# Optimization experiments

Hardware: AMD Instinct MI355X
Metric: run time of the kernel (lower is better)

## Reference

```python
import jax, jax.numpy as jnp
import numpy as np

D_MODEL = 2048
N_HEADS = 16
D_HEAD = 128
B = 2
S = 2048


def setup_inputs() -> dict:
    key = jax.random.key(0)
    ks = jax.random.split(key, 9)
    sc_in = 1.0 / np.sqrt(D_MODEL)
    sc_hd = 1.0 / np.sqrt(N_HEADS * D_HEAD)
    return {
        "x": jax.random.normal(ks[0], (B, S, D_MODEL), dtype=jnp.float32),
        "Wq": jax.random.normal(ks[1], (D_MODEL, N_HEADS * D_HEAD), dtype=jnp.float32) * sc_in,
        "bq": jax.random.normal(ks[2], (N_HEADS * D_HEAD,), dtype=jnp.float32) * 0.01,
        "Wk": jax.random.normal(ks[3], (D_MODEL, N_HEADS * D_HEAD), dtype=jnp.float32) * sc_in,
        "bk": jax.random.normal(ks[4], (N_HEADS * D_HEAD,), dtype=jnp.float32) * 0.01,
        "Wv": jax.random.normal(ks[5], (D_MODEL, N_HEADS * D_HEAD), dtype=jnp.float32) * sc_in,
        "bv": jax.random.normal(ks[6], (N_HEADS * D_HEAD,), dtype=jnp.float32) * 0.01,
        "Wo": jax.random.normal(ks[7], (N_HEADS * D_HEAD, D_MODEL), dtype=jnp.float32) * sc_hd,
        "bo": jax.random.normal(ks[8], (D_MODEL,), dtype=jnp.float32) * 0.01,
    }


def reference(x, Wq, bq, Wk, bk, Wv, bv, Wo, bo):
    b, s, _ = x.shape
    # projections -> [b, s, h, d] -> [b, h, s, d]
    q = (x @ Wq + bq).reshape(b, s, N_HEADS, D_HEAD).transpose(0, 2, 1, 3)
    k = (x @ Wk + bk).reshape(b, s, N_HEADS, D_HEAD).transpose(0, 2, 1, 3)
    v = (x @ Wv + bv).reshape(b, s, N_HEADS, D_HEAD).transpose(0, 2, 1, 3)
    scale = 1.0 / jnp.sqrt(jnp.asarray(D_HEAD, dtype=x.dtype))
    scores = jnp.einsum("bhsd,bhtd->bhst", q, k) * scale  # [b,h,s,s]
    causal = jnp.triu(jnp.ones((s, s), dtype=bool), k=1)
    scores = jnp.where(causal, jnp.asarray(-jnp.inf, dtype=scores.dtype), scores)
    attn = jax.nn.softmax(scores, axis=-1)
    ctx = jnp.einsum("bhst,bhtd->bhsd", attn, v)  # [b,h,s,d]
    ctx = ctx.transpose(0, 2, 1, 3).reshape(b, s, N_HEADS * D_HEAD)
    return ctx @ Wo + bo
```

## Files before the change

### kernel.cpp

```cpp
#include <hip/hip_runtime.h>
#include <hip/hip_bf16.h>
#include <stdint.h>

#define S_LEN  2048
#define DMODEL 2048
#define NHEADS 16
#define DHEAD  128
#define NBATCH 2
#define MROWS  (NBATCH * S_LEN)

typedef __bf16 bf16_t;
typedef __bf16 bf16x8 __attribute__((ext_vector_type(8)));
typedef float  f32x4  __attribute__((ext_vector_type(4)));
typedef float  f32x16 __attribute__((ext_vector_type(16)));

#define MFMA_BF16(A, B, C) __builtin_amdgcn_mfma_f32_16x16x32_bf16((A), (B), (C), 0, 0, 0)
#define MFMA32(A, B, C)    __builtin_amdgcn_mfma_f32_32x32x16_bf16((A), (B), (C), 0, 0, 0)

__device__ __forceinline__ void gload_lds16(const void* g, void* l) {
  __builtin_amdgcn_global_load_lds(
      (__attribute__((address_space(1))) uint32_t*)(uintptr_t)g,
      (__attribute__((address_space(3))) uint32_t*)l,
      16, 0, 0);
}

__device__ __forceinline__ unsigned pk2(float lo, float hi) {
  const unsigned short a = __builtin_bit_cast(unsigned short, (bf16_t)lo);
  const unsigned short b = __builtin_bit_cast(unsigned short, (bf16_t)hi);
  return (unsigned)a | ((unsigned)b << 16);
}

__global__ __launch_bounds__(256) void cast_kernel(const float* __restrict__ X,
                                                   bf16_t* __restrict__ Xb) {
  const int i = blockIdx.x * 256 + threadIdx.x;
  const f32x4 a = ((const f32x4*)X)[2 * i];
  const f32x4 b = ((const f32x4*)X)[2 * i + 1];
  bf16x8 o;
#pragma unroll
  for (int j = 0; j < 4; ++j) { o[j] = (bf16_t)a[j]; o[j + 4] = (bf16_t)b[j]; }
  ((bf16x8*)Xb)[i] = o;
}

__global__ __launch_bounds__(256) void transpose_cast(
    const float* __restrict__ W0, const float* __restrict__ W1,
    const float* __restrict__ W2, const float* __restrict__ W3,
    bf16_t* __restrict__ T0, bf16_t* __restrict__ T1,
    bf16_t* __restrict__ T2, bf16_t* __restrict__ T3) {
  const float* W; bf16_t* T;
  switch (blockIdx.z) {
    case 0:  W = W0; T = T0; break;
    case 1:  W = W1; T = T1; break;
    case 2:  W = W2; T = T2; break;
    default: W = W3; T = T3; break;
  }
  __shared__ float tile[64][65];
  const int r0 = blockIdx.y * 64;
  const int c0 = blockIdx.x * 64;
  const int tx = threadIdx.x & 63;
  const int ty = threadIdx.x >> 6;
#pragma unroll
  for (int i = 0; i < 16; ++i) {
    const int r = ty + i * 4;
    tile[r][tx] = W[(size_t)(r0 + r) * DMODEL + c0 + tx];
  }
  __syncthreads();
#pragma unroll
  for (int i = 0; i < 16; ++i) {
    const int r = ty + i * 4;
    T[(size_t)(c0 + r) * DMODEL + r0 + tx] = (bf16_t)tile[tx][r];
  }
}

__global__ __launch_bounds__(256) void transpose_v(const bf16_t* __restrict__ V,
                                                   bf16_t* __restrict__ VT) {
  __shared__ bf16_t tile[64 * 64];
  const int bh = blockIdx.z;
  const int s0 = blockIdx.x * 64;
  const int d0 = blockIdx.y * 64;
  const bf16_t* src = V + ((size_t)bh * S_LEN + s0) * DHEAD + d0;
#pragma unroll
  for (int i = 0; i < 2; ++i) {
    const int v = threadIdx.x + i * 256;
    const int r = v >> 3, ch = v & 7;
    *(bf16x8*)&tile[r * 64 + ((ch ^ ((r >> 3) & 7)) << 3)] =
        *(const bf16x8*)(src + (size_t)r * DHEAD + ch * 8);
  }
  __syncthreads();
  bf16_t* dst = VT + ((size_t)bh * DHEAD + d0) * S_LEN + s0;
#pragma unroll
  for (int i = 0; i < 2; ++i) {
    const int v = threadIdx.x + i * 256;
    const int d = v >> 3, j = v & 7;
    bf16x8 o;
#pragma unroll
    for (int e = 0; e < 8; ++e) {
      const int row = j * 8 + e;
      o[e] = tile[row * 64 + (((d >> 3) ^ j) << 3) + (d & 7)];
    }
    *(bf16x8*)(dst + (size_t)d * S_LEN + j * 8) = o;
  }
}

template <int MODE>
__device__ __forceinline__ void gemm_body(const bf16_t* __restrict__ A,
                                          const bf16_t* __restrict__ Bt,
                                          const float* __restrict__ bias,
                                          void* __restrict__ out) {
  __shared__ bf16_t lds[128 * 32 * 2];
  const int tid  = threadIdx.x;
  const int lane = tid & 63;
  const int w    = tid >> 6;
  const int g    = lane >> 4;
  const int l16  = lane & 15;
  const int m0   = blockIdx.y * 128;
  const int n0   = blockIdx.x * 128;
  const int wm   = w >> 1, wn = w & 1;

  f32x4 acc[4][4];
#pragma unroll
  for (int i = 0; i < 4; ++i)
#pragma unroll
    for (int j = 0; j < 4; ++j) acc[i][j] = (f32x4){0.f, 0.f, 0.f, 0.f};

  const bf16_t* src   = (w < 2) ? A : Bt;
  const int rowbase   = (w < 2) ? m0 : n0;
  char* ldsst         = (char*)lds + (w >= 2 ? 8192 : 0);
  const char* lA      = (const char*)lds;
  const char* lB      = (const char*)lds + 8192;

  for (int kt = 0; kt < DMODEL; kt += 32) {
#pragma unroll
    for (int it = 0; it < 4; ++it) {
      const int c   = (w & 1) * 256 + it * 64 + lane;
      const int row = c >> 2;
      const int q4  = (c & 3) ^ (row & 3);
      gload_lds16(src + (size_t)(rowbase + row) * DMODEL + kt + q4 * 8,
                  ldsst + ((w & 1) * 256 + it * 64) * 16);
    }
    asm volatile("s_waitcnt vmcnt(0)" ::: "memory");
    __syncthreads();

    bf16x8 af[4], bfr[4];
#pragma unroll
    for (int i = 0; i < 4; ++i) {
      const int row = wm * 64 + i * 16 + l16;
      af[i] = *(const bf16x8*)(lA + row * 64 + ((g * 16) ^ ((row & 3) << 4)));
    }
#pragma unroll
    for (int j = 0; j < 4; ++j) {
      const int row = wn * 64 + j * 16 + l16;
      bfr[j] = *(const bf16x8*)(lB + row * 64 + ((g * 16) ^ ((row & 3) << 4)));
    }
#pragma unroll
    for (int i = 0; i < 4; ++i)
#pragma unroll
      for (int j = 0; j < 4; ++j)
        acc[i][j] = MFMA_BF16(af[i], bfr[j], acc[i][j]);
    __syncthreads();
  }

#pragma unroll
  for (int i = 0; i < 4; ++i) {
#pragma unroll
    for (int j = 0; j < 4; ++j) {
      const int n    = n0 + wn * 64 + j * 16 + l16;
      const float bb = bias[n];
#pragma unroll
      for (int r = 0; r < 4; ++r) {
        const int m   = m0 + wm * 64 + i * 16 + g * 4 + r;
        const float v = acc[i][j][r] + bb;
        if (MODE == 0) {
          const int b = m >> 11, s = m & (S_LEN - 1);
          const int h = n >> 7,  d = n & (DHEAD - 1);
          ((bf16_t*)out)[((size_t)(b * NHEADS + h) * S_LEN + s) * DHEAD + d] = (bf16_t)v;
        } else {
          ((float*)out)[(size_t)m * DMODEL + n] = v;
        }
      }
    }
  }
}

__global__ __launch_bounds__(256, 2) void gemm_qkv(
    const bf16_t* __restrict__ Xb,
    const bf16_t* __restrict__ WqT, const bf16_t* __restrict__ WkT,
    const bf16_t* __restrict__ WvT,
    const float* __restrict__ bq, const float* __restrict__ bk,
    const float* __restrict__ bv,
    bf16_t* __restrict__ Qg, bf16_t* __restrict__ Kg, bf16_t* __restrict__ Vg) {
  const bf16_t* Bt; const float* bias; bf16_t* out;
  if (blockIdx.z == 0)      { Bt = WqT; bias = bq; out = Qg; }
  else if (blockIdx.z == 1) { Bt = WkT; bias = bk; out = Kg; }
  else                      { Bt = WvT; bias = bv; out = Vg; }
  gemm_body<0>(Xb, Bt, bias, out);
}

__global__ __launch_bounds__(256, 2) void gemm_out(
    const bf16_t* __restrict__ Ctx, const bf16_t* __restrict__ WoT,
    const float* __restrict__ bo, float* __restrict__ out) {
  gemm_body<1>(Ctx, WoT, bo, out);
}

#define KLDS_BYTES (64 * 272)
#define VLDS_BYTES (128 * 144)
#define BUF_BYTES  (KLDS_BYTES + VLDS_BYTES)

__global__ __launch_bounds__(256, 2) void attn_kernel(
    const bf16_t* __restrict__ Qg, const bf16_t* __restrict__ Kg,
    const bf16_t* __restrict__ VTg, bf16_t* __restrict__ ctx) {
  __shared__ __align__(16) char ldsbuf[2][BUF_BYTES];
  __shared__ float lbuf[4][32];

  const int tid  = threadIdx.x;
  const int lane = tid & 63;
  const int w    = tid >> 6;
  const int l31  = lane & 31;
  const int hi   = lane >> 5;

  const int id   = blockIdx.x;
  const int bh   = id & 31;
  const int jraw = id >> 5;
  const int j    = (jraw < 8) ? jraw : 23 - jraw;
  const int q0   = j * 128;
  const int qw   = q0 + w * 32;
  const int tq   = (qw + 31) >> 6;
  const int NT   = (q0 + 128) >> 6;

  const size_t bho = (size_t)bh * S_LEN * DHEAD;
  const bf16_t* Qb  = Qg + bho;
  const bf16_t* Kb  = Kg + bho;
  const bf16_t* VTb = VTg + bho;

  bf16x8 qreg[8];
#pragma unroll
  for (int s = 0; s < 8; ++s)
    qreg[s] = *(const bf16x8*)(Qb + (size_t)(qw + l31) * DHEAD + s * 16 + hi * 8);

  f32x16 oacc[4];
#pragma unroll
  for (int d0 = 0; d0 < 4; ++d0)
#pragma unroll
    for (int e = 0; e < 16; ++e) oacc[d0][e] = 0.f;

  float m = -1e30f, lsum = 0.f;
  const float sc2 = 0.12751751135f;

  bf16x8 kst[4], vst[4];
#pragma unroll
  for (int i = 0; i < 4; ++i) {
    const int c = tid + i * 256;
    kst[i] = *(const bf16x8*)(Kb + (size_t)(c >> 4) * DHEAD + (c & 15) * 8);
    vst[i] = *(const bf16x8*)(VTb + (size_t)(c >> 3) * S_LEN + (c & 7) * 8);
  }
#pragma unroll
  for (int i = 0; i < 4; ++i) {
    const int c  = tid + i * 256;
    const int kr = c >> 4, kc = c & 15;
    *(bf16x8*)(ldsbuf[0] + kr * 272 + ((kc ^ ((kr >> 3) & 3)) << 4)) = kst[i];
    const int vr = c >> 3, vc = c & 7;
    *(bf16x8*)(ldsbuf[0] + KLDS_BYTES + vr * 144 + ((vc ^ ((vr >> 3) & 3)) << 4)) = vst[i];
  }
  __syncthreads();

  for (int t = 0; t < NT; ++t) {
    const int kt = t << 6;
    const char* bK = ldsbuf[t & 1];
    const char* bV = bK + KLDS_BYTES;
    const bool hn = (t + 1 < NT);
    if (hn) {
#pragma unroll
      for (int i = 0; i < 4; ++i) {
        const int c = tid + i * 256;
        kst[i] = *(const bf16x8*)(Kb + (size_t)(kt + 64 + (c >> 4)) * DHEAD + (c & 15) * 8);
        vst[i] = *(const bf16x8*)(VTb + (size_t)(c >> 3) * S_LEN + kt + 64 + (c & 7) * 8);
      }
    }

    if (t <= tq) {
      f32x16 stt[2];
#pragma unroll
      for (int kh = 0; kh < 2; ++kh)
#pragma unroll
        for (int e = 0; e < 16; ++e) stt[kh][e] = 0.f;
#pragma unroll
      for (int kh = 0; kh < 2; ++kh) {
        const int row = kh * 32 + l31;
        const char* rb = bK + row * 272;
        const int swz = ((row >> 3) & 3) << 4;
#pragma unroll
        for (int s = 0; s < 8; ++s) {
          const bf16x8 kf = *(const bf16x8*)(rb + ((((s << 1) | hi) << 4) ^ swz));
          stt[kh] = MFMA32(kf, qreg[s], stt[kh]);
        }
      }
      if (t == tq) {
        const int qg = qw + l31;
#pragma unroll
        for (int kh = 0; kh < 2; ++kh)
#pragma unroll
          for (int r = 0; r < 16; ++r) {
            const int kv = kt + kh * 32 + (r & 3) + 8 * (r >> 2) + 4 * hi;
            stt[kh][r] = (kv > qg) ? -1e30f : stt[kh][r];
          }
      }
      float pm = stt[0][0];
#pragma unroll
      for (int kh = 0; kh < 2; ++kh)
#pragma unroll
        for (int r = 0; r < 16; ++r)
          if (kh | r) pm = fmaxf(pm, stt[kh][r]);
      pm = fmaxf(pm, __shfl_xor(pm, 32));
      const float pmax = pm * sc2;
      if (!__all(pmax <= m + 8.f)) {
        const float mn   = fmaxf(m, pmax);
        const float corr = __builtin_amdgcn_exp2f(m - mn);
        m = mn;
        lsum *= corr;
        if (!hi) lbuf[w][l31] = corr;
#pragma unroll
        for (int r = 0; r < 16; ++r) {
          const float cr = lbuf[w][(r & 3) + 8 * (r >> 2) + 4 * hi];
#pragma unroll
          for (int d0 = 0; d0 < 4; ++d0) oacc[d0][r] *= cr;
        }
      }
      float rs = 0.f;
#pragma unroll
      for (int kh = 0; kh < 2; ++kh)
#pragma unroll
        for (int r = 0; r < 16; ++r) {
          const float p = __builtin_amdgcn_exp2f(__builtin_fmaf(stt[kh][r], sc2, -m));
          stt[kh][r] = p;
          rs += p;
        }
      rs += __shfl_xor(rs, 32);
      lsum += rs;
      unsigned pw_[2][8];
#pragma unroll
      for (int kh = 0; kh < 2; ++kh)
#pragma unroll
        for (int jj = 0; jj < 8; ++jj)
          pw_[kh][jj] = pk2(stt[kh][2 * jj], stt[kh][2 * jj + 1]);
      bf16x8 pa[4];
#pragma unroll
      for (int kh = 0; kh < 2; ++kh)
#pragma unroll
        for (int c2 = 0; c2 < 2; ++c2) {
          const unsigned o0 = pw_[kh][4 * c2 + 0], o1 = pw_[kh][4 * c2 + 1];
          const unsigned o2 = pw_[kh][4 * c2 + 2], o3 = pw_[kh][4 * c2 + 3];
          const unsigned p0 = (unsigned)__shfl_xor((int)o0, 32);
          const unsigned p1 = (unsigned)__shfl_xor((int)o1, 32);
          const unsigned p2 = (unsigned)__shfl_xor((int)o2, 32);
          const unsigned p3 = (unsigned)__shfl_xor((int)o3, 32);
          union { unsigned u[4]; bf16x8 v; } uu;
          uu.u[0] = hi ? p2 : o0;
          uu.u[1] = hi ? p3 : o1;
          uu.u[2] = hi ? o2 : p0;
          uu.u[3] = hi ? o3 : p1;
          pa[2 * kh + c2] = uu.v;
        }
#pragma unroll
      for (int d0 = 0; d0 < 4; ++d0) {
        const int row = d0 * 32 + l31;
        const char* rb = bV + row * 144;
        const int swz = ((row >> 3) & 3) << 4;
#pragma unroll
        for (int ks = 0; ks < 4; ++ks) {
          const bf16x8 vb = *(const bf16x8*)(rb + ((((ks << 1) | hi) << 4) ^ swz));
          oacc[d0] = MFMA32(pa[ks], vb, oacc[d0]);
        }
      }
    }
    __syncthreads();
    if (hn) {
      char* nB = ldsbuf[(t + 1) & 1];
#pragma unroll
      for (int i = 0; i < 4; ++i) {
        const int c  = tid + i * 256;
        const int kr = c >> 4, kc = c & 15;
        *(bf16x8*)(nB + kr * 272 + ((kc ^ ((kr >> 3) & 3)) << 4)) = kst[i];
        const int vr = c >> 3, vc = c & 7;
        *(bf16x8*)(nB + KLDS_BYTES + vr * 144 + ((vc ^ ((vr >> 3) & 3)) << 4)) = vst[i];
      }
    }
    __syncthreads();
  }

  if (!hi) lbuf[w][l31] = 1.0f / lsum;
  const int b = bh >> 4, h = bh & 15;
#pragma unroll
  for (int r = 0; r < 16; ++r) {
    const int cro = (r & 3) + 8 * (r >> 2) + 4 * hi;
    const float li = lbuf[w][cro];
    const size_t base = ((size_t)(b * S_LEN + qw + cro)) * DMODEL + h * DHEAD;
#pragma unroll
    for (int d0 = 0; d0 < 4; ++d0)
      ctx[base + d0 * 32 + l31] = (bf16_t)(oacc[d0][r] * li);
  }
}

extern "C" void kernel_launch(void* const* d_in, const int* in_sizes, int n_in,
                              void* d_out, int out_size, void* d_ws, size_t ws_size,
                              hipStream_t stream) {
  const float* x  = (const float*)d_in[0];
  const float* Wq = (const float*)d_in[1];
  const float* bq = (const float*)d_in[2];
  const float* Wk = (const float*)d_in[3];
  const float* bk = (const float*)d_in[4];
  const float* Wv = (const float*)d_in[5];
  const float* bv = (const float*)d_in[6];
  const float* Wo = (const float*)d_in[7];
  const float* bo = (const float*)d_in[8];

  char* ws = (char*)d_ws;
  const size_t MB = 1ull << 20;
  bf16_t* Xb  = (bf16_t*)(ws + 0);
  bf16_t* VTg = (bf16_t*)(ws + 0);
  bf16_t* WqT = (bf16_t*)(ws + 16 * MB);
  bf16_t* WkT = (bf16_t*)(ws + 24 * MB);
  bf16_t* WvT = (bf16_t*)(ws + 32 * MB);
  bf16_t* WoT = (bf16_t*)(ws + 40 * MB);
  bf16_t* Qg  = (bf16_t*)(ws + 48 * MB);
  bf16_t* Kg  = (bf16_t*)(ws + 64 * MB);
  bf16_t* Vg  = (bf16_t*)(ws + 80 * MB);
  bf16_t* Ctx = (bf16_t*)(ws + 96 * MB);
  if (ws_size < 112 * MB) return;

  cast_kernel<<<dim3(MROWS * DMODEL / (256 * 8)), 256, 0, stream>>>(x, Xb);
  transpose_cast<<<dim3(32, 32, 4), 256, 0, stream>>>(Wq, Wk, Wv, Wo, WqT, WkT, WvT, WoT);
  gemm_qkv<<<dim3(DMODEL / 128, MROWS / 128, 3), 256, 0, stream>>>(
      Xb, WqT, WkT, WvT, bq, bk, bv, Qg, Kg, Vg);
  transpose_v<<<dim3(32, 2, 32), 256, 0, stream>>>(Vg, VTg);
  attn_kernel<<<dim3(512), 256, 0, stream>>>(Qg, Kg, VTg, Ctx);
  gemm_out<<<dim3(DMODEL / 128, MROWS / 128), 256, 0, stream>>>(Ctx, WoT, bo, (float*)d_out);
}
```

Measured before the change: 266.0 us.

## Rewrite projection GEMMs as 8-wave 128x256 tiles with double-buffered LDS prefetch

Replaces the single-buffered 128x128, 4-wave GEMM body with an 8-wave kernel covering 128x256 output tiles at K-step 64. Global-to-LDS loads for the next tile are issued between the two MFMA phases, so memory traffic overlaps compute; raw s_barrier calls and explicit waitcnt replace the full syncthreads, and s_setprio raises priority around the MFMA blocks. The wider tile cuts re-reads of A. In exchange it uses 96KB of LDS per block, which limits occupancy to about one block per CU, and relies on hand-tuned vmcnt counts being correct.

```diff
diff --git a/kernel.cpp b/kernel.cpp
--- a/kernel.cpp
+++ b/kernel.cpp
@@ -102,19 +102,20 @@
 }
 
 template <int MODE>
-__device__ __forceinline__ void gemm_body(const bf16_t* __restrict__ A,
-                                          const bf16_t* __restrict__ Bt,
-                                          const float* __restrict__ bias,
-                                          void* __restrict__ out) {
-  __shared__ bf16_t lds[128 * 32 * 2];
+__device__ __forceinline__ void gemm8_body(const bf16_t* __restrict__ A,
+                                           const bf16_t* __restrict__ Bt,
+                                           const float* __restrict__ bias,
+                                           void* __restrict__ out) {
+  __shared__ __align__(16) char lds8[2 * 49152];
   const int tid  = threadIdx.x;
   const int lane = tid & 63;
   const int w    = tid >> 6;
   const int g    = lane >> 4;
   const int l16  = lane & 15;
+  const int wm   = w >> 2;
+  const int wn   = w & 3;
   const int m0   = blockIdx.y * 128;
-  const int n0   = blockIdx.x * 128;
-  const int wm   = w >> 1, wn = w & 1;
+  const int n0   = blockIdx.x * 256;
 
   f32x4 acc[4][4];
 #pragma unroll
@@ -122,41 +123,83 @@
 #pragma unroll
     for (int j = 0; j < 4; ++j) acc[i][j] = (f32x4){0.f, 0.f, 0.f, 0.f};
 
-  const bf16_t* src   = (w < 2) ? A : Bt;
-  const int rowbase   = (w < 2) ? m0 : n0;
-  char* ldsst         = (char*)lds + (w >= 2 ? 8192 : 0);
-  const char* lA      = (const char*)lds;
-  const char* lB      = (const char*)lds + 8192;
-
-  for (int kt = 0; kt < DMODEL; kt += 32) {
-#pragma unroll
-    for (int it = 0; it < 4; ++it) {
-      const int c   = (w & 1) * 256 + it * 64 + lane;
-      const int row = c >> 2;
-      const int q4  = (c & 3) ^ (row & 3);
-      gload_lds16(src + (size_t)(rowbase + row) * DMODEL + kt + q4 * 8,
-                  ldsst + ((w & 1) * 256 + it * 64) * 16);
-    }
-    asm volatile("s_waitcnt vmcnt(0)" ::: "memory");
-    __syncthreads();
-
-    bf16x8 af[4], bfr[4];
+  const int st_r0 = tid >> 3;
+  const int st_ch = tid & 7;
+
+  auto stage = [&](int tile, int r) {
+    if (tile >= DMODEL / 64) return;
+    const int kt = tile << 6;
+    char* db = lds8 + (tile & 1) * 49152 + r * 16384 + w * 1024;
+    const bf16_t* sb = (r == 0) ? (A + (size_t)m0 * DMODEL + kt)
+                                : (Bt + (size_t)(n0 + ((r - 1) << 7)) * DMODEL + kt);
+#pragma unroll
+    for (int jj = 0; jj < 2; ++jj) {
+      const int row = jj * 64 + st_r0;
+      gload_lds16(sb + (size_t)row * DMODEL + ((st_ch ^ (row & 7)) << 3),
+                  db + jj * 8192);
+    }
+  };
+
+  stage(0, 0); stage(0, 1); stage(0, 2); stage(1, 0);
+  asm volatile("s_waitcnt vmcnt(2)" ::: "memory");
+  __builtin_amdgcn_s_barrier();
+
+#pragma unroll 2
+  for (int t = 0; t < DMODEL / 64; ++t) {
+    const char* cb = lds8 + (t & 1) * 49152;
+    bf16x8 af[4][2], b0[2][2], b1[2][2];
 #pragma unroll
     for (int i = 0; i < 4; ++i) {
       const int row = wm * 64 + i * 16 + l16;
-      af[i] = *(const bf16x8*)(lA + row * 64 + ((g * 16) ^ ((row & 3) << 4)));
-    }
-#pragma unroll
-    for (int j = 0; j < 4; ++j) {
-      const int row = wn * 64 + j * 16 + l16;
-      bfr[j] = *(const bf16x8*)(lB + row * 64 + ((g * 16) ^ ((row & 3) << 4)));
-    }
+      const char* rp = cb + row * 128;
+#pragma unroll
+      for (int ks = 0; ks < 2; ++ks)
+        af[i][ks] = *(const bf16x8*)(rp + ((((ks << 2) | g) ^ (row & 7)) << 4));
+    }
+#pragma unroll
+    for (int j = 0; j < 2; ++j) {
+      const int row = (wn & 1) * 64 + j * 16 + l16;
+      const char* rp = cb + 16384 + (wn >> 1) * 16384 + row * 128;
+#pragma unroll
+      for (int ks = 0; ks < 2; ++ks)
+        b0[j][ks] = *(const bf16x8*)(rp + ((((ks << 2) | g) ^ (row & 7)) << 4));
+    }
+    stage(t + 1, 1); stage(t + 1, 2);
+    __builtin_amdgcn_s_barrier();
+    asm volatile("s_waitcnt lgkmcnt(0)" ::: "memory");
+    __builtin_amdgcn_s_setprio(1);
 #pragma unroll
     for (int i = 0; i < 4; ++i)
 #pragma unroll
-      for (int j = 0; j < 4; ++j)
-        acc[i][j] = MFMA_BF16(af[i], bfr[j], acc[i][j]);
-    __syncthreads();
+      for (int j = 0; j < 2; ++j) {
+        acc[i][j] = MFMA_BF16(af[i][0], b0[j][0], acc[i][j]);
+        acc[i][j] = MFMA_BF16(af[i][1], b0[j][1], acc[i][j]);
+      }
+    __builtin_amdgcn_s_setprio(0);
+    __builtin_amdgcn_s_barrier();
+#pragma unroll
+    for (int j = 0; j < 2; ++j) {
+      const int row = (wn & 1) * 64 + (j + 2) * 16 + l16;
+      const char* rp = cb + 16384 + (wn >> 1) * 16384 + row * 128;
+#pragma unroll
+      for (int ks = 0; ks < 2; ++ks)
+        b1[j][ks] = *(const bf16x8*)(rp + ((((ks << 2) | g) ^ (row & 7)) << 4));
+    }
+    stage(t + 2, 0);
+    __builtin_amdgcn_s_barrier();
+    asm volatile("s_waitcnt lgkmcnt(0)" ::: "memory");
+    __builtin_amdgcn_s_setprio(1);
+#pragma unroll
+    for (int i = 0; i < 4; ++i)
+#pragma unroll
+      for (int j = 0; j < 2; ++j) {
+        acc[i][j + 2] = MFMA_BF16(af[i][0], b1[j][0], acc[i][j + 2]);
+        acc[i][j + 2] = MFMA_BF16(af[i][1], b1[j][1], acc[i][j + 2]);
+      }
+    __builtin_amdgcn_s_setprio(0);
+    if (t < DMODEL / 64 - 2) asm volatile("s_waitcnt vmcnt(2)" ::: "memory");
+    else                     asm volatile("s_waitcnt vmcnt(0)" ::: "memory");
+    __builtin_amdgcn_s_barrier();
   }
 
 #pragma unroll
@@ -181,7 +224,7 @@
   }
 }
 
-__global__ __launch_bounds__(256, 2) void gemm_qkv(
+__global__ __launch_bounds__(512, 2) void gemm_qkv(
     const bf16_t* __restrict__ Xb,
     const bf16_t* __restrict__ WqT, const bf16_t* __restrict__ WkT,
     const bf16_t* __restrict__ WvT,
@@ -192,13 +235,13 @@
   if (blockIdx.z == 0)      { Bt = WqT; bias = bq; out = Qg; }
   else if (blockIdx.z == 1) { Bt = WkT; bias = bk; out = Kg; }
   else                      { Bt = WvT; bias = bv; out = Vg; }
-  gemm_body<0>(Xb, Bt, bias, out);
-}
-
-__global__ __launch_bounds__(256, 2) void gemm_out(
+  gemm8_body<0>(Xb, Bt, bias, out);
+}
+
+__global__ __launch_bounds__(512, 2) void gemm_out(
     const bf16_t* __restrict__ Ctx, const bf16_t* __restrict__ WoT,
     const float* __restrict__ bo, float* __restrict__ out) {
-  gemm_body<1>(Ctx, WoT, bo, out);
+  gemm8_body<1>(Ctx, WoT, bo, out);
 }
 
 #define KLDS_BYTES (64 * 272)
@@ -428,9 +471,9 @@
 
   cast_kernel<<<dim3(MROWS * DMODEL / (256 * 8)), 256, 0, stream>>>(x, Xb);
   transpose_cast<<<dim3(32, 32, 4), 256, 0, stream>>>(Wq, Wk, Wv, Wo, WqT, WkT, WvT, WoT);
-  gemm_qkv<<<dim3(DMODEL / 128, MROWS / 128, 3), 256, 0, stream>>>(
+  gemm_qkv<<<dim3(DMODEL / 256, MROWS / 128, 3), 512, 0, stream>>>(
       Xb, WqT, WkT, WvT, bq, bk, bv, Qg, Kg, Vg);
   transpose_v<<<dim3(32, 2, 32), 256, 0, stream>>>(Vg, VTg);
   attn_kernel<<<dim3(512), 256, 0, stream>>>(Qg, Kg, VTg, Ctx);
-  gemm_out<<<dim3(DMODEL / 128, MROWS / 128), 256, 0, stream>>>(Ctx, WoT, bo, (float*)d_out);
-}
+  gemm_out<<<dim3(DMODEL / 256, MROWS / 128), 512, 0, stream>>>(Ctx, WoT, bo, (float*)d_out);
+}
```

Measured after the change: 235.1 us. -11.6%, faster.
